# Optimization experiments

Measured on AMD Instinct MI355X. Metric: run time of the kernel, lower is better.

The kernel has to match this reference:

```python
import jax, jax.numpy as jnp
import numpy as np

B, T, D, H = 512, 2048, 8, 64


def _lstm_layer(x, w_ih, w_hh, b_ih, b_hh):
    """x: [B,T,D_in] -> h_seq: [B,T,H]. PyTorch gate order i,f,g,o."""
    Bn = x.shape[0]
    Hn = w_hh.shape[1]
    # Precompute input contributions for all timesteps: [T,B,4H]
    xg = jnp.einsum('btd,gd->tbg', x, w_ih) + (b_ih + b_hh)

    def step(carry, xt):
        h, c = carry
        gates = xt + h @ w_hh.T  # [B,4H]
        i, f, g, o = jnp.split(gates, 4, axis=-1)
        i = jax.nn.sigmoid(i)
        f = jax.nn.sigmoid(f)
        g = jnp.tanh(g)
        o = jax.nn.sigmoid(o)
        c = f * c + i * g
        h = o * jnp.tanh(c)
        return (h, c), h

    h0 = jnp.zeros((Bn, Hn), x.dtype)
    c0 = jnp.zeros((Bn, Hn), x.dtype)
    (_, _), h_seq = jax.lax.scan(step, (h0, c0), xg)
    return jnp.transpose(h_seq, (1, 0, 2))  # [B,T,H]


def setup_inputs() -> dict:
    key = jax.random.key(0)
    ks = jax.random.split(key, 11)
    s = 1.0 / np.sqrt(H)
    return {
        'x': jax.random.normal(ks[0], (B, T, D), jnp.float32),
        'w_ih0': jax.random.normal(ks[1], (4 * H, D), jnp.float32) * s,
        'w_hh0': jax.random.normal(ks[2], (4 * H, H), jnp.float32) * s,
        'b_ih0': jax.random.normal(ks[3], (4 * H,), jnp.float32) * s,
        'b_hh0': jax.random.normal(ks[4], (4 * H,), jnp.float32) * s,
        'w_ih1': jax.random.normal(ks[5], (4 * H, H), jnp.float32) * s,
        'w_hh1': jax.random.normal(ks[6], (4 * H, H), jnp.float32) * s,
        'b_ih1': jax.random.normal(ks[7], (4 * H,), jnp.float32) * s,
        'b_hh1': jax.random.normal(ks[8], (4 * H,), jnp.float32) * s,
        'w_out': jax.random.normal(ks[9], (1, H), jnp.float32) * s,
        'b_out': jax.random.normal(ks[10], (1,), jnp.float32) * s,
    }


def reference(x, w_ih0, w_hh0, b_ih0, b_hh0, w_ih1, w_hh1, b_ih1, b_hh1, w_out, b_out):
    h1 = _lstm_layer(x, w_ih0, w_hh0, b_ih0, b_hh0)   # [B,T,H]
    h2 = _lstm_layer(h1, w_ih1, w_hh1, b_ih1, b_hh1)  # [B,T,H]
    last = h2[:, -1, :]                               # [B,H]
    return last @ w_out.T + b_out                     # [B,1]
```

## Files before the change

### kernel.cpp

```cpp
#include <hip/hip_runtime.h>

#define BB 512
#define TT 2048
#define DD 8
#define HH 64
#define NB 4
#define NBLK (BB / NB)

typedef _Float16 f16x8 __attribute__((ext_vector_type(8)));
typedef __fp16   fp16x2 __attribute__((ext_vector_type(2)));
typedef float    f32x4 __attribute__((ext_vector_type(4)));

__device__ __forceinline__ float rcpf(float x) { return __builtin_amdgcn_rcpf(x); }
__device__ __forceinline__ float sigm(float x) { return rcpf(1.0f + __expf(-x)); }
__device__ __forceinline__ float tanh_fast(float x) {
  return 1.0f - 2.0f * rcpf(__expf(2.0f * x) + 1.0f);
}
__device__ __forceinline__ f16x8 cvt8(const float* __restrict__ p) {
  f16x8 r;
#pragma unroll
  for (int e = 0; e < 8; ++e) r[e] = (_Float16)p[e];
  return r;
}

__global__ void __launch_bounds__(512, 1)
lstm2_mfma(const float* __restrict__ x,
           const float* __restrict__ w_ih0, const float* __restrict__ w_hh0,
           const float* __restrict__ b_ih0, const float* __restrict__ b_hh0,
           const float* __restrict__ w_ih1, const float* __restrict__ w_hh1,
           const float* __restrict__ b_ih1, const float* __restrict__ b_hh1,
           const float* __restrict__ w_out, const float* __restrict__ b_out,
           float* __restrict__ out)
{
  const int tid  = threadIdx.x;
  const int lane = tid & 63;
  const int wq   = tid >> 6;
  const int lay  = wq >> 2;
  const int q    = wq & 3;
  const int lg   = lane >> 4;
  const int ar   = lane & 15;
  const int col  = lane & 3;
  const int rsel = (lane >> 2) & 3;
  const int tile = blockIdx.x;

  __shared__ __align__(16) unsigned char h0buf[2][16][128];
  __shared__ __align__(16) unsigned char h1buf[2][16][128];
  __shared__ float hout[HH][NB];

  {
    float* z0 = (float*)h0buf;
    float* z1 = (float*)h1buf;
    for (int i = tid; i < (int)(sizeof(h0buf) / 4); i += 512) { z0[i] = 0.f; z1[i] = 0.f; }
  }

  f16x8 a_x[4];
  f16x8 aU[4][2];
  f16x8 aV[4][2];
  f32x4 bC[4];
#pragma unroll
  for (int ti = 0; ti < 4; ++ti) {
    const int tile_m = q + 4 * ti;
    const int ga     = 16 * tile_m + ar;
    f16x8 zf = {};
    a_x[ti] = zf;
    if (lay == 0) {
      if (lg == 0) a_x[ti] = cvt8(w_ih0 + ga * DD);
#pragma unroll
      for (int kf = 0; kf < 2; ++kf) {
        aU[ti][kf] = cvt8(w_hh0 + ga * HH + kf * 32 + lg * 8);
        aV[ti][kf] = zf;
      }
#pragma unroll
      for (int r = 0; r < 4; ++r) {
        const int gc = 16 * tile_m + 4 * lg + r;
        bC[ti][r] = b_ih0[gc] + b_hh0[gc];
      }
    } else {
#pragma unroll
      for (int kf = 0; kf < 2; ++kf) {
        const int off = ga * HH + kf * 32 + lg * 8;
        aU[ti][kf] = cvt8(w_ih1 + off);
        aV[ti][kf] = cvt8(w_hh1 + off);
      }
#pragma unroll
      for (int r = 0; r < 4; ++r) {
        const int gc = 16 * tile_m + 4 * lg + r;
        bC[ti][r] = b_ih1[gc] + b_hh1[gc];
      }
    }
  }

  const int xr = tile * NB + (ar < NB ? ar : 0);
  const float4* xrow = (const float4*)(x + (size_t)xr * TT * DD);
  float4 xA = make_float4(0, 0, 0, 0), xB = make_float4(0, 0, 0, 0);
  if (lay == 0) { xA = xrow[0]; xB = xrow[1]; }

  float cv  = 0.0f;
  float hv1 = 0.0f;

  const int kk   = 16 * q + 4 * (lane >> 4) + rsel;
  const int pubB = 16 * ((kk >> 3) ^ col) + 2 * (kk & 7);
  const int rd0 = 16 * ((0 + lg) ^ (ar & 7));
  const int rd1 = 16 * ((4 + lg) ^ (ar & 7));

  __syncthreads();

  for (int t = 0; t <= TT; ++t) {
    const int p  = t & 1;
    const int rp = p ^ 1;

    if (lay == 0) {
      const f16x8 hf0_0 = *(const f16x8*)&h0buf[rp][ar][rd0];
      const f16x8 hf0_1 = *(const f16x8*)&h0buf[rp][ar][rd1];

      f16x8 xf = {};
      if (lg == 0 && ar < NB) {
        union { fp16x2 h2[4]; f16x8 v; } X;
        X.h2[0] = __builtin_amdgcn_cvt_pkrtz(xA.x, xA.y);
        X.h2[1] = __builtin_amdgcn_cvt_pkrtz(xA.z, xA.w);
        X.h2[2] = __builtin_amdgcn_cvt_pkrtz(xB.x, xB.y);
        X.h2[3] = __builtin_amdgcn_cvt_pkrtz(xB.z, xB.w);
        xf = X.v;
      }
      {
        const int tn = (t + 1 < TT) ? (t + 1) : (TT - 1);
        xA = xrow[2 * tn];
        xB = xrow[2 * tn + 1];
      }

      f32x4 acc[4];
#pragma unroll
      for (int ti = 0; ti < 4; ++ti)
        acc[ti] = __builtin_amdgcn_mfma_f32_16x16x32_f16(a_x[ti], xf, bC[ti], 0, 0, 0);
#pragma unroll
      for (int ti = 0; ti < 4; ++ti)
        acc[ti] = __builtin_amdgcn_mfma_f32_16x16x32_f16(aU[ti][0], hf0_0, acc[ti], 0, 0, 0);
#pragma unroll
      for (int ti = 0; ti < 4; ++ti)
        acc[ti] = __builtin_amdgcn_mfma_f32_16x16x32_f16(aU[ti][1], hf0_1, acc[ti], 0, 0, 0);

      f32x4 ga;
#pragma unroll
      for (int ti = 0; ti < 4; ++ti) {
        const int s0 = __builtin_amdgcn_ds_swizzle(__float_as_int(acc[ti][0]), 0x0013);
        const int s1 = __builtin_amdgcn_ds_swizzle(__float_as_int(acc[ti][1]), 0x0013);
        const int s2 = __builtin_amdgcn_ds_swizzle(__float_as_int(acc[ti][2]), 0x0013);
        const int s3 = __builtin_amdgcn_ds_swizzle(__float_as_int(acc[ti][3]), 0x0013);
        const int v01 = (rsel & 1) ? s1 : s0;
        const int v23 = (rsel & 1) ? s3 : s2;
        ga[ti] = __int_as_float((rsel & 2) ? v23 : v01);
      }

      const float i_ = sigm(ga[0]);
      const float f_ = sigm(ga[1]);
      const float g_ = tanh_fast(ga[2]);
      const float o_ = sigm(ga[3]);
      cv = fmaf(f_, cv, i_ * g_);
      const float h = o_ * tanh_fast(cv);
      *(_Float16*)&h0buf[p][col][pubB] = (_Float16)h;
    } else {
      const f16x8 hf0_0 = *(const f16x8*)&h0buf[rp][ar][rd0];
      const f16x8 hf0_1 = *(const f16x8*)&h0buf[rp][ar][rd1];
      const f16x8 hf1_0 = *(const f16x8*)&h1buf[rp][ar][rd0];
      const f16x8 hf1_1 = *(const f16x8*)&h1buf[rp][ar][rd1];

      f32x4 acd[4];
#pragma unroll
      for (int ti = 0; ti < 4; ++ti)
        acd[ti] = __builtin_amdgcn_mfma_f32_16x16x32_f16(aU[ti][0], hf0_0, bC[ti], 0, 0, 0);
#pragma unroll
      for (int ti = 0; ti < 4; ++ti)
        acd[ti] = __builtin_amdgcn_mfma_f32_16x16x32_f16(aU[ti][1], hf0_1, acd[ti], 0, 0, 0);
#pragma unroll
      for (int ti = 0; ti < 4; ++ti)
        acd[ti] = __builtin_amdgcn_mfma_f32_16x16x32_f16(aV[ti][0], hf1_0, acd[ti], 0, 0, 0);
#pragma unroll
      for (int ti = 0; ti < 4; ++ti)
        acd[ti] = __builtin_amdgcn_mfma_f32_16x16x32_f16(aV[ti][1], hf1_1, acd[ti], 0, 0, 0);

      if (t != 0) {
        f32x4 ga;
#pragma unroll
        for (int ti = 0; ti < 4; ++ti) {
          const int s0 = __builtin_amdgcn_ds_swizzle(__float_as_int(acd[ti][0]), 0x0013);
          const int s1 = __builtin_amdgcn_ds_swizzle(__float_as_int(acd[ti][1]), 0x0013);
          const int s2 = __builtin_amdgcn_ds_swizzle(__float_as_int(acd[ti][2]), 0x0013);
          const int s3 = __builtin_amdgcn_ds_swizzle(__float_as_int(acd[ti][3]), 0x0013);
          const int v01 = (rsel & 1) ? s1 : s0;
          const int v23 = (rsel & 1) ? s3 : s2;
          ga[ti] = __int_as_float((rsel & 2) ? v23 : v01);
        }

        const float i_ = sigm(ga[0]);
        const float f_ = sigm(ga[1]);
        const float g_ = tanh_fast(ga[2]);
        const float o_ = sigm(ga[3]);
        cv = fmaf(f_, cv, i_ * g_);
        hv1 = o_ * tanh_fast(cv);
        *(_Float16*)&h1buf[p][col][pubB] = (_Float16)hv1;
      }
    }

    asm volatile("s_waitcnt lgkmcnt(0)" ::: "memory");
    __builtin_amdgcn_s_barrier();
    __builtin_amdgcn_sched_barrier(0);
  }

  if (lay == 1) hout[kk][col] = hv1;
  __syncthreads();
  if (tid < NB) {
    float v = b_out[0];
    for (int k = 0; k < HH; ++k) v = fmaf(hout[k][tid], w_out[k], v);
    out[tile * NB + tid] = v;
  }
}

extern "C" void kernel_launch(void* const* d_in, const int* in_sizes, int n_in,
                              void* d_out, int out_size, void* d_ws, size_t ws_size,
                              hipStream_t stream) {
  const float* x     = (const float*)d_in[0];
  const float* w_ih0 = (const float*)d_in[1];
  const float* w_hh0 = (const float*)d_in[2];
  const float* b_ih0 = (const float*)d_in[3];
  const float* b_hh0 = (const float*)d_in[4];
  const float* w_ih1 = (const float*)d_in[5];
  const float* w_hh1 = (const float*)d_in[6];
  const float* b_ih1 = (const float*)d_in[7];
  const float* b_hh1 = (const float*)d_in[8];
  const float* w_out = (const float*)d_in[9];
  const float* b_out = (const float*)d_in[10];
  float* out = (float*)d_out;

  lstm2_mfma<<<dim3(NBLK), dim3(512), 0, stream>>>(
      x, w_ih0, w_hh0, b_ih0, b_hh0,
      w_ih1, w_hh1, b_ih1, b_hh1,
      w_out, b_out, out);
}
```

Before: 1.249 ms.

## Split LSTM timestep into two barrier phases to overlap layer MFMAs with activations

Each timestep now has two barrier-separated phases. In the first, layer 0 runs its recurrent MFMAs while layer 1 applies activations to gates computed in the previous phase. In the second, layer 0 applies its activations and precomputes the next input projection while layer 1 runs its MFMAs. This moves the x-projection MFMA off the critical path and staggers the two layers' matrix and elementwise work so they run concurrently. The cost is twice as many block barriers per step, a deeper layer-1 pipeline lag, and a final drain step after the loop.

Measured after the change: 1.392 ms. 11.5% more time.

```diff
diff --git a/kernel.cpp b/kernel.cpp
--- a/kernel.cpp
+++ b/kernel.cpp
@@ -22,6 +22,13 @@
   for (int e = 0; e < 8; ++e) r[e] = (_Float16)p[e];
   return r;
 }
+
+#define DSBAR()                                          \
+  do {                                                   \
+    asm volatile("s_waitcnt lgkmcnt(0)" ::: "memory");   \
+    __builtin_amdgcn_s_barrier();                        \
+    __builtin_amdgcn_sched_barrier(0);                   \
+  } while (0)
 
 __global__ void __launch_bounds__(512, 1)
 lstm2_mfma(const float* __restrict__ x,
@@ -100,8 +107,28 @@
 
   const int kk   = 16 * q + 4 * (lane >> 4) + rsel;
   const int pubB = 16 * ((kk >> 3) ^ col) + 2 * (kk & 7);
-  const int rd0 = 16 * ((0 + lg) ^ (ar & 7));
-  const int rd1 = 16 * ((4 + lg) ^ (ar & 7));
+  const int rd0  = 16 * ((0 + lg) ^ (ar & 7));
+  const int rd1  = 16 * ((4 + lg) ^ (ar & 7));
+
+  f32x4 xpre[4];
+  if (lay == 0) {
+    f16x8 xf = {};
+    if (lg == 0 && ar < NB) {
+      union { fp16x2 h2[4]; f16x8 v; } X;
+      X.h2[0] = __builtin_amdgcn_cvt_pkrtz(xA.x, xA.y);
+      X.h2[1] = __builtin_amdgcn_cvt_pkrtz(xA.z, xA.w);
+      X.h2[2] = __builtin_amdgcn_cvt_pkrtz(xB.x, xB.y);
+      X.h2[3] = __builtin_amdgcn_cvt_pkrtz(xB.z, xB.w);
+      xf = X.v;
+    }
+#pragma unroll
+    for (int ti = 0; ti < 4; ++ti)
+      xpre[ti] = __builtin_amdgcn_mfma_f32_16x16x32_f16(a_x[ti], xf, bC[ti], 0, 0, 0);
+  }
+
+  f32x4 gatesR[4];
+#pragma unroll
+  for (int ti = 0; ti < 4; ++ti) gatesR[ti] = (f32x4){0.f, 0.f, 0.f, 0.f};
 
   __syncthreads();
 
@@ -112,6 +139,59 @@
     if (lay == 0) {
       const f16x8 hf0_0 = *(const f16x8*)&h0buf[rp][ar][rd0];
       const f16x8 hf0_1 = *(const f16x8*)&h0buf[rp][ar][rd1];
+#pragma unroll
+      for (int ti = 0; ti < 4; ++ti)
+        gatesR[ti] = __builtin_amdgcn_mfma_f32_16x16x32_f16(aU[ti][0], hf0_0, xpre[ti], 0, 0, 0);
+#pragma unroll
+      for (int ti = 0; ti < 4; ++ti)
+        gatesR[ti] = __builtin_amdgcn_mfma_f32_16x16x32_f16(aU[ti][1], hf0_1, gatesR[ti], 0, 0, 0);
+      {
+        const int tn = (t + 1 < TT) ? (t + 1) : (TT - 1);
+        xA = xrow[2 * tn];
+        xB = xrow[2 * tn + 1];
+      }
+    } else if (t >= 2) {
+      f32x4 ga;
+#pragma unroll
+      for (int ti = 0; ti < 4; ++ti) {
+        const int s0 = __builtin_amdgcn_ds_swizzle(__float_as_int(gatesR[ti][0]), 0x0013);
+        const int s1 = __builtin_amdgcn_ds_swizzle(__float_as_int(gatesR[ti][1]), 0x0013);
+        const int s2 = __builtin_amdgcn_ds_swizzle(__float_as_int(gatesR[ti][2]), 0x0013);
+        const int s3 = __builtin_amdgcn_ds_swizzle(__float_as_int(gatesR[ti][3]), 0x0013);
+        const int v01 = (rsel & 1) ? s1 : s0;
+        const int v23 = (rsel & 1) ? s3 : s2;
+        ga[ti] = __int_as_float((rsel & 2) ? v23 : v01);
+      }
+      const float i_ = sigm(ga[0]);
+      const float f_ = sigm(ga[1]);
+      const float g_ = tanh_fast(ga[2]);
+      const float o_ = sigm(ga[3]);
+      cv = fmaf(f_, cv, i_ * g_);
+      hv1 = o_ * tanh_fast(cv);
+      *(_Float16*)&h1buf[p][col][pubB] = (_Float16)hv1;
+    }
+
+    DSBAR();
+
+    if (lay == 0) {
+      f32x4 ga;
+#pragma unroll
+      for (int ti = 0; ti < 4; ++ti) {
+        const int s0 = __builtin_amdgcn_ds_swizzle(__float_as_int(gatesR[ti][0]), 0x0013);
+        const int s1 = __builtin_amdgcn_ds_swizzle(__float_as_int(gatesR[ti][1]), 0x0013);
+        const int s2 = __builtin_amdgcn_ds_swizzle(__float_as_int(gatesR[ti][2]), 0x0013);
+        const int s3 = __builtin_amdgcn_ds_swizzle(__float_as_int(gatesR[ti][3]), 0x0013);
+        const int v01 = (rsel & 1) ? s1 : s0;
+        const int v23 = (rsel & 1) ? s3 : s2;
+        ga[ti] = __int_as_float((rsel & 2) ? v23 : v01);
+      }
+      const float i_ = sigm(ga[0]);
+      const float f_ = sigm(ga[1]);
+      const float g_ = tanh_fast(ga[2]);
+      const float o_ = sigm(ga[3]);
+      cv = fmaf(f_, cv, i_ * g_);
+      const float h = o_ * tanh_fast(cv);
+      *(_Float16*)&h0buf[p][col][pubB] = (_Float16)h;
 
       f16x8 xf = {};
       if (lg == 0 && ar < NB) {
@@ -122,92 +202,53 @@
         X.h2[3] = __builtin_amdgcn_cvt_pkrtz(xB.z, xB.w);
         xf = X.v;
       }
-      {
-        const int tn = (t + 1 < TT) ? (t + 1) : (TT - 1);
-        xA = xrow[2 * tn];
-        xB = xrow[2 * tn + 1];
-      }
-
-      f32x4 acc[4];
-#pragma unroll
-      for (int ti = 0; ti < 4; ++ti)
-        acc[ti] = __builtin_amdgcn_mfma_f32_16x16x32_f16(a_x[ti], xf, bC[ti], 0, 0, 0);
-#pragma unroll
-      for (int ti = 0; ti < 4; ++ti)
-        acc[ti] = __builtin_amdgcn_mfma_f32_16x16x32_f16(aU[ti][0], hf0_0, acc[ti], 0, 0, 0);
-#pragma unroll
-      for (int ti = 0; ti < 4; ++ti)
-        acc[ti] = __builtin_amdgcn_mfma_f32_16x16x32_f16(aU[ti][1], hf0_1, acc[ti], 0, 0, 0);
-
-      f32x4 ga;
-#pragma unroll
-      for (int ti = 0; ti < 4; ++ti) {
-        const int s0 = __builtin_amdgcn_ds_swizzle(__float_as_int(acc[ti][0]), 0x0013);
-        const int s1 = __builtin_amdgcn_ds_swizzle(__float_as_int(acc[ti][1]), 0x0013);
-        const int s2 = __builtin_amdgcn_ds_swizzle(__float_as_int(acc[ti][2]), 0x0013);
-        const int s3 = __builtin_amdgcn_ds_swizzle(__float_as_int(acc[ti][3]), 0x0013);
-        const int v01 = (rsel & 1) ? s1 : s0;
-        const int v23 = (rsel & 1) ? s3 : s2;
-        ga[ti] = __int_as_float((rsel & 2) ? v23 : v01);
-      }
-
-      const float i_ = sigm(ga[0]);
-      const float f_ = sigm(ga[1]);
-      const float g_ = tanh_fast(ga[2]);
-      const float o_ = sigm(ga[3]);
-      cv = fmaf(f_, cv, i_ * g_);
-      const float h = o_ * tanh_fast(cv);
-      *(_Float16*)&h0buf[p][col][pubB] = (_Float16)h;
+#pragma unroll
+      for (int ti = 0; ti < 4; ++ti)
+        xpre[ti] = __builtin_amdgcn_mfma_f32_16x16x32_f16(a_x[ti], xf, bC[ti], 0, 0, 0);
     } else {
       const f16x8 hf0_0 = *(const f16x8*)&h0buf[rp][ar][rd0];
       const f16x8 hf0_1 = *(const f16x8*)&h0buf[rp][ar][rd1];
-      const f16x8 hf1_0 = *(const f16x8*)&h1buf[rp][ar][rd0];
-      const f16x8 hf1_1 = *(const f16x8*)&h1buf[rp][ar][rd1];
-
-      f32x4 acd[4];
-#pragma unroll
-      for (int ti = 0; ti < 4; ++ti)
-        acd[ti] = __builtin_amdgcn_mfma_f32_16x16x32_f16(aU[ti][0], hf0_0, bC[ti], 0, 0, 0);
-#pragma unroll
-      for (int ti = 0; ti < 4; ++ti)
-        acd[ti] = __builtin_amdgcn_mfma_f32_16x16x32_f16(aU[ti][1], hf0_1, acd[ti], 0, 0, 0);
-#pragma unroll
-      for (int ti = 0; ti < 4; ++ti)
-        acd[ti] = __builtin_amdgcn_mfma_f32_16x16x32_f16(aV[ti][0], hf1_0, acd[ti], 0, 0, 0);
-#pragma unroll
-      for (int ti = 0; ti < 4; ++ti)
-        acd[ti] = __builtin_amdgcn_mfma_f32_16x16x32_f16(aV[ti][1], hf1_1, acd[ti], 0, 0, 0);
-
-      if (t != 0) {
-        f32x4 ga;
-#pragma unroll
-        for (int ti = 0; ti < 4; ++ti) {
-          const int s0 = __builtin_amdgcn_ds_swizzle(__float_as_int(acd[ti][0]), 0x0013);
-          const int s1 = __builtin_amdgcn_ds_swizzle(__float_as_int(acd[ti][1]), 0x0013);
-          const int s2 = __builtin_amdgcn_ds_swizzle(__float_as_int(acd[ti][2]), 0x0013);
-          const int s3 = __builtin_amdgcn_ds_swizzle(__float_as_int(acd[ti][3]), 0x0013);
-          const int v01 = (rsel & 1) ? s1 : s0;
-          const int v23 = (rsel & 1) ? s3 : s2;
-          ga[ti] = __int_as_float((rsel & 2) ? v23 : v01);
-        }
-
-        const float i_ = sigm(ga[0]);
-        const float f_ = sigm(ga[1]);
-        const float g_ = tanh_fast(ga[2]);
-        const float o_ = sigm(ga[3]);
-        cv = fmaf(f_, cv, i_ * g_);
-        hv1 = o_ * tanh_fast(cv);
-        *(_Float16*)&h1buf[p][col][pubB] = (_Float16)hv1;
-      }
-    }
-
-    asm volatile("s_waitcnt lgkmcnt(0)" ::: "memory");
-    __builtin_amdgcn_s_barrier();
-    __builtin_amdgcn_sched_barrier(0);
-  }
-
-  if (lay == 1) hout[kk][col] = hv1;
+      const f16x8 hf1_0 = *(const f16x8*)&h1buf[p][ar][rd0];
+      const f16x8 hf1_1 = *(const f16x8*)&h1buf[p][ar][rd1];
+#pragma unroll
+      for (int ti = 0; ti < 4; ++ti)
+        gatesR[ti] = __builtin_amdgcn_mfma_f32_16x16x32_f16(aU[ti][0], hf0_0, bC[ti], 0, 0, 0);
+#pragma unroll
+      for (int ti = 0; ti < 4; ++ti)
+        gatesR[ti] = __builtin_amdgcn_mfma_f32_16x16x32_f16(aU[ti][1], hf0_1, gatesR[ti], 0, 0, 0);
+#pragma unroll
+      for (int ti = 0; ti < 4; ++ti)
+        gatesR[ti] = __builtin_amdgcn_mfma_f32_16x16x32_f16(aV[ti][0], hf1_0, gatesR[ti], 0, 0, 0);
+#pragma unroll
+      for (int ti = 0; ti < 4; ++ti)
+        gatesR[ti] = __builtin_amdgcn_mfma_f32_16x16x32_f16(aV[ti][1], hf1_1, gatesR[ti], 0, 0, 0);
+    }
+
+    DSBAR();
+  }
+
+  if (lay == 1) {
+    f32x4 ga;
+#pragma unroll
+    for (int ti = 0; ti < 4; ++ti) {
+      const int s0 = __builtin_amdgcn_ds_swizzle(__float_as_int(gatesR[ti][0]), 0x0013);
+      const int s1 = __builtin_amdgcn_ds_swizzle(__float_as_int(gatesR[ti][1]), 0x0013);
+      const int s2 = __builtin_amdgcn_ds_swizzle(__float_as_int(gatesR[ti][2]), 0x0013);
+      const int s3 = __builtin_amdgcn_ds_swizzle(__float_as_int(gatesR[ti][3]), 0x0013);
+      const int v01 = (rsel & 1) ? s1 : s0;
+      const int v23 = (rsel & 1) ? s3 : s2;
+      ga[ti] = __int_as_float((rsel & 2) ? v23 : v01);
+    }
+    const float i_ = sigm(ga[0]);
+    const float f_ = sigm(ga[1]);
+    const float g_ = tanh_fast(ga[2]);
+    const float o_ = sigm(ga[3]);
+    cv = fmaf(f_, cv, i_ * g_);
+    hv1 = o_ * tanh_fast(cv);
+    hout[kk][col] = hv1;
+  }
   __syncthreads();
+
   if (tid < NB) {
     float v = b_out[0];
     for (int k = 0; k < HH; ++k) v = fmaf(hout[k][tid], w_out[k], v);
```
